# Performance work log

Hardware: AMD Instinct MI355X
Metric: run time of the kernel (lower is better)

The kernel has to match this reference:

```python
import jax, jax.numpy as jnp
import numpy as np

D_MODEL = 1024
NUM_HEADS = 16
D_HEAD = D_MODEL // NUM_HEADS
THETA = 10000.0
NEG_INF = -1e9


def apply_rope(x, theta=THETA):
    # x: (..., S, Dh) with interleaved pairs (2i, 2i+1)
    S, Dh = x.shape[-2], x.shape[-1]
    inv_freq = 1.0 / (theta ** (jnp.arange(0, Dh, 2, dtype=jnp.float32) / Dh))  # (Dh/2,)
    ang = jnp.arange(S, dtype=jnp.float32)[:, None] * inv_freq[None, :]          # (S, Dh/2)
    cos, sin = jnp.cos(ang), jnp.sin(ang)
    x1 = x[..., 0::2]
    x2 = x[..., 1::2]
    r1 = x1 * cos - x2 * sin
    r2 = x1 * sin + x2 * cos
    # interleave back
    return jnp.stack([r1, r2], axis=-1).reshape(x.shape)


def setup_inputs() -> dict:
    key = jax.random.key(0)
    ks = jax.random.split(key, 5)
    B, S = 2, 2048
    scale = 1.0 / np.sqrt(D_MODEL)
    return {
        "x": jax.random.normal(ks[0], (B, S, D_MODEL), dtype=jnp.float32),
        "Wq": jax.random.normal(ks[1], (D_MODEL, D_MODEL), dtype=jnp.float32) * scale,
        "Wk": jax.random.normal(ks[2], (D_MODEL, D_MODEL), dtype=jnp.float32) * scale,
        "Wv": jax.random.normal(ks[3], (D_MODEL, D_MODEL), dtype=jnp.float32) * scale,
        "Wo": jax.random.normal(ks[4], (D_MODEL, D_MODEL), dtype=jnp.float32) * scale,
    }


def reference(x, Wq, Wk, Wv, Wo):
    B, S, _ = x.shape
    def split_heads(t):
        return t.reshape(B, S, NUM_HEADS, D_HEAD).transpose(0, 2, 1, 3)  # (B,H,S,Dh)
    # nn.Linear(bias=False): y = x @ W.T
    Q = split_heads(x @ Wq.T)
    K = split_heads(x @ Wk.T)
    V = split_heads(x @ Wv.T)
    Q = apply_rope(Q)
    K = apply_rope(K)
    scale = 1.0 / jnp.sqrt(jnp.asarray(D_HEAD, dtype=x.dtype))
    scores = jnp.einsum("bhqd,bhkd->bhqk", Q, K) * scale  # (B,H,S,S)
    causal = jnp.tril(jnp.ones((S, S), dtype=bool))
    scores = jnp.where(causal, scores, NEG_INF)
    attn = jax.nn.softmax(scores, axis=-1)
    out = jnp.einsum("bhqk,bhkd->bhqd", attn, V)
    out = out.transpose(0, 2, 1, 3).reshape(B, S, D_MODEL)
    return out @ Wo.T
```

## Files before the change

kernel.cpp:

```cpp
#include <hip/hip_runtime.h>
#include <hip/hip_bf16.h>
#include <stdint.h>

typedef __attribute__((ext_vector_type(8))) short bf8;
typedef __attribute__((ext_vector_type(4))) float f4;
typedef __attribute__((ext_vector_type(16))) float f16f;
typedef __attribute__((ext_vector_type(4))) unsigned int u32x4;

#define MFMA16(a, b, c) __builtin_amdgcn_mfma_f32_16x16x32_bf16((a), (b), (c), 0, 0, 0)
#define MFMA32(a, b, c) __builtin_amdgcn_mfma_f32_32x32x16_bf16((a), (b), (c), 0, 0, 0)

static __device__ __forceinline__ short f2b(float f) {
  uint32_t x = __float_as_uint(f);
  x += 0x7fffu + ((x >> 16) & 1u);
  return (short)(x >> 16);
}

static __device__ __forceinline__ uint32_t cvtpk(float lo, float hi) {
  uint32_t r;
  asm("v_cvt_pk_bf16_f32 %0, %1, %2" : "=v"(r) : "v"(lo), "v"(hi));
  return r;
}

static __device__ __forceinline__ bf8 mk_bf8(uint32_t w0, uint32_t w1,
                                             uint32_t w2, uint32_t w3) {
  union { u32x4 u; bf8 b; } t;
  t.u = (u32x4){w0, w1, w2, w3};
  return t.b;
}

static __device__ __forceinline__ void gload16(const short* g, void* l) {
  __builtin_amdgcn_global_load_lds(
      (const __attribute__((address_space(1))) void*)g,
      (__attribute__((address_space(3))) void*)l, 16, 0, 0);
}

__global__ void convert_kernel(const float* __restrict__ x,
                               const float* __restrict__ wq, const float* __restrict__ wk,
                               const float* __restrict__ wv, const float* __restrict__ wo,
                               short* __restrict__ xb, short* __restrict__ Wb,
                               float2* __restrict__ tab) {
  const int bid = blockIdx.x;
  if (bid >= 4096) {
    const int t = (bid - 4096) * 256 + threadIdx.x;
    const int s = t >> 5, i = t & 31;
    const float inv = powf(10000.0f, -(float)i * (1.0f / 32.0f));
    const float ang = (float)s * inv;
    float sv, cv;
    sincosf(ang, &sv, &cv);
    tab[t] = make_float2(cv, sv);
    return;
  }
  const size_t i = ((size_t)bid * 256 + threadIdx.x) * 8;
  const float* __restrict__ src;
  short* __restrict__ dst;
  if (i < 4194304u) {
    src = x + i;
    dst = xb + i;
  } else {
    const size_t j = i - 4194304u;
    const int z = (int)(j >> 20);
    const size_t o = j & 1048575u;
    src = (z == 0 ? wq : z == 1 ? wk : z == 2 ? wv : wo) + o;
    dst = Wb + j;
  }
  const float4 a = *(const float4*)src;
  const float4 b = *(const float4*)(src + 4);
  bf8 v;
  v[0] = f2b(a.x); v[1] = f2b(a.y); v[2] = f2b(a.z); v[3] = f2b(a.w);
  v[4] = f2b(b.x); v[5] = f2b(b.y); v[6] = f2b(b.z); v[7] = f2b(b.w);
  *(bf8*)dst = v;
}

template <int MODE>
__launch_bounds__(256, 2)
__global__ void gemm_kernel(const short* __restrict__ Ab, const short* __restrict__ Wb,
                            short* __restrict__ Qo, short* __restrict__ Ko,
                            short* __restrict__ VTo, float* __restrict__ Fo,
                            const float2* __restrict__ rope) {
  constexpr int K = 1024;
  const int bm = blockIdx.x, bn = blockIdx.y;
  const int z = (MODE == 0) ? blockIdx.z : 3;
  const short* __restrict__ Bb = Wb + ((size_t)z << 20);

  __shared__ short As[128 * 64];
  __shared__ short Bs[128 * 64];

  const int tid = threadIdx.x;
  const int lane = tid & 63;
  const int wave = tid >> 6;
  const int wr = wave >> 1, wc = wave & 1;
  const int lg = lane >> 4, lr = lane & 15;

  f4 acc[4][4];
#pragma unroll
  for (int i = 0; i < 4; i++)
#pragma unroll
    for (int j = 0; j < 4; j++) {
      acc[i][j][0] = 0.f; acc[i][j][1] = 0.f;
      acc[i][j][2] = 0.f; acc[i][j][3] = 0.f;
    }

  const int kc = tid & 7;
  const int srow = tid >> 3;
  const int kcs = (kc ^ (srow & 7)) * 8;
  char* const Asw = (char*)As + wave * 1024;
  char* const Bsw = (char*)Bs + wave * 1024;

  for (int k0 = 0; k0 < K; k0 += 64) {
#pragma unroll
    for (int i = 0; i < 4; i++) {
      const int row = srow + i * 32;
      gload16(Ab + (size_t)(bm * 128 + row) * K + k0 + kcs, Asw + i * 4096);
      gload16(Bb + (size_t)(bn * 128 + row) * K + k0 + kcs, Bsw + i * 4096);
    }
    __syncthreads();
#pragma unroll
    for (int kk = 0; kk < 2; kk++) {
      bf8 af[4], bb[4];
#pragma unroll
      for (int mi = 0; mi < 4; mi++) {
        const int row = wr * 64 + mi * 16 + lr;
        const int lb = (row * 128 + kk * 64 + lg * 16) ^ ((row & 7) << 4);
        af[mi] = *(const bf8*)((const char*)As + lb);
      }
#pragma unroll
      for (int ni = 0; ni < 4; ni++) {
        const int row = wc * 64 + ni * 16 + lr;
        const int lb = (row * 128 + kk * 64 + lg * 16) ^ ((row & 7) << 4);
        bb[ni] = *(const bf8*)((const char*)Bs + lb);
      }
#pragma unroll
      for (int mi = 0; mi < 4; mi++)
#pragma unroll
        for (int ni = 0; ni < 4; ni++)
          acc[mi][ni] = MFMA16(af[mi], bb[ni], acc[mi][ni]);
    }
    __syncthreads();
  }

  if (MODE == 1) {
#pragma unroll
    for (int mi = 0; mi < 4; mi++) {
      const int m0 = bm * 128 + wr * 64 + mi * 16 + lg * 4;
#pragma unroll
      for (int ni = 0; ni < 4; ni++) {
        const int n = bn * 128 + wc * 64 + ni * 16 + lr;
#pragma unroll
        for (int r = 0; r < 4; r++)
          Fo[(size_t)(m0 + r) * 1024 + n] = acc[mi][ni][r];
      }
    }
    return;
  }

  if (z == 2) {
#pragma unroll
    for (int mi = 0; mi < 4; mi++) {
      const int m0 = bm * 128 + wr * 64 + mi * 16 + lg * 4;
      const int b = m0 >> 11, s0 = m0 & 2047;
#pragma unroll
      for (int ni = 0; ni < 4; ni++) {
        const int n = bn * 128 + wc * 64 + ni * 16 + lr;
        const int h = n >> 6, d = n & 63;
        ushort4 pk;
        pk.x = (unsigned short)f2b(acc[mi][ni][0]);
        pk.y = (unsigned short)f2b(acc[mi][ni][1]);
        pk.z = (unsigned short)f2b(acc[mi][ni][2]);
        pk.w = (unsigned short)f2b(acc[mi][ni][3]);
        ((ushort4*)VTo)[((size_t)(b * 16 + h) * 32 + (s0 >> 6)) * 1024 +
                        (((s0 & 63) >> 2) << 6) + d] = pk;
      }
    }
  } else {
    const float qscale = (z == 0) ? 0.18033688011112042f : 1.0f;
#pragma unroll
    for (int mi = 0; mi < 4; mi++) {
      const int m0 = bm * 128 + wr * 64 + mi * 16 + lg * 4;
      const int b = m0 >> 11, s0 = m0 & 2047;
#pragma unroll
      for (int ni = 0; ni < 4; ni++) {
        const int n = bn * 128 + wc * 64 + ni * 16 + lr;
        const int h = n >> 6, d = n & 63;
        const float sgn = (d & 1) ? 1.0f : -1.0f;
#pragma unroll
        for (int r = 0; r < 4; r++) {
          const float v = acc[mi][ni][r];
          const float p = __shfl_xor(v, 1);
          const int s = s0 + r;
          const float2 cs = rope[(s << 5) + (d >> 1)];
          const short res = f2b((v * cs.x + sgn * p * cs.y) * qscale);
          if (z == 0) {
            Qo[((size_t)(b * 16 + h) * 2048 + s) * 64 + d] = res;
          } else {
            Ko[(((size_t)(b * 16 + h) * 32 + (s >> 6)) << 12) +
               ((((d >> 3) << 6) + (s & 63)) << 3) + (d & 7)] = res;
          }
        }
      }
    }
  }
}

__launch_bounds__(256, 2)
__global__ void attn_kernel(const short* __restrict__ Qg, const short* __restrict__ K2,
                            const short* __restrict__ V2, short* __restrict__ AO) {
  const int id = blockIdx.x;
  const int xcd = id & 7;
  const int rest = id >> 3;
  const int bh = xcd * 4 + (rest & 3);
  const int j = 15 - (rest >> 2);
  const int tid = threadIdx.x;
  const int lane = tid & 63, wave = tid >> 6;
  const int l31 = lane & 31, hi = lane >> 5;
  const short* __restrict__ Qp = Qg + ((size_t)bh << 17);
  const short* __restrict__ KR = K2 + ((size_t)bh << 17);
  const short* __restrict__ VR = V2 + ((size_t)bh << 17);

  __shared__ short KB[2][2][4096];
  __shared__ short VB[2][2][4096];

  const int t = 4 * j + wave;
  const int qbase = t << 5;
  const int nR = j + 1;

#define STG(buf, kb_)                                                             \
  do {                                                                            \
    _Pragma("unroll") for (int h_ = 0; h_ < 2; h_++) {                            \
      const short* kr_ = KR + ((size_t)((kb_) * 2 + h_) << 12);                   \
      const short* vr_ = VR + ((size_t)((kb_) * 2 + h_) << 12);                   \
      gload16(kr_ + (size_t)(wave * 64 + lane) * 8, (char*)KB[buf][h_] + wave * 1024);          \
      gload16(kr_ + (size_t)(256 + wave * 64 + lane) * 8, (char*)KB[buf][h_] + 4096 + wave * 1024); \
      gload16(vr_ + (size_t)(wave * 64 + lane) * 8, (char*)VB[buf][h_] + wave * 1024);          \
      gload16(vr_ + (size_t)(256 + wave * 64 + lane) * 8, (char*)VB[buf][h_] + 4096 + wave * 1024); \
    }                                                                             \
  } while (0)

  bf8 qf[4];
#pragma unroll
  for (int ks = 0; ks < 4; ks++)
    qf[ks] = *(const bf8*)(Qp + (size_t)(qbase + l31) * 64 + ks * 16 + hi * 8);

  f16f o0, o1;
#pragma unroll
  for (int i = 0; i < 16; i++) { o0[i] = 0.f; o1[i] = 0.f; }
  float mrun = -1e30f, lsum = 0.f;

  STG(0, 0);
  __syncthreads();

  for (int kb = 0; kb < nR; kb++) {
    const int cur = kb & 1;

    if (kb + 1 < nR) STG(cur ^ 1, kb + 1);

#pragma unroll
    for (int h = 0; h < 2; h++) {
      const int kvbh = kb * 128 + 64 * h;
      if (kvbh < qbase + 32) {
        const char* Kc = (const char*)KB[cur][h];
        const char* Vc = (const char*)VB[cur][h];

        f16f st0, st1;
#pragma unroll
        for (int i = 0; i < 16; i++) { st0[i] = 0.f; st1[i] = 0.f; }
        __builtin_amdgcn_s_setprio(1);
#pragma unroll
        for (int ks = 0; ks < 4; ks++) {
          const bf8 k0f = *(const bf8*)(Kc + (2 * ks + hi) * 1024 + l31 * 16);
          const bf8 k1f = *(const bf8*)(Kc + (2 * ks + hi) * 1024 + (32 + l31) * 16);
          st0 = MFMA32(k0f, qf[ks], st0);
          st1 = MFMA32(k1f, qf[ks], st1);
        }
        __builtin_amdgcn_s_setprio(0);

        if (kvbh + 63 > qbase) {
          const int q = qbase + l31;
#pragma unroll
          for (int reg = 0; reg < 16; reg++) {
            const int kv = kvbh + (reg & 3) + 8 * (reg >> 2) + 4 * hi;
            if (kv > q) st0[reg] = -1e9f;
            if (kv + 32 > q) st1[reg] = -1e9f;
          }
        }

        float m0 = fmaxf(st0[0], st1[0]);
#pragma unroll
        for (int reg = 1; reg < 16; reg++) m0 = fmaxf(m0, fmaxf(st0[reg], st1[reg]));

        if (__any(m0 - mrun > 8.0f)) {
          m0 = fmaxf(m0, __shfl_xor(m0, 32));
          const float mn = fmaxf(mrun, m0);
          const float corr = __builtin_amdgcn_exp2f(mrun - mn);
          mrun = mn;
          lsum *= corr;
#pragma unroll
          for (int reg = 0; reg < 16; reg++) {
            const int qo = (reg & 3) + 8 * (reg >> 2) + 4 * hi;
            const float co = __shfl(corr, qo);
            o0[reg] *= co;
            o1[reg] *= co;
          }
        }

#pragma unroll
        for (int reg = 0; reg < 16; reg++) {
          st0[reg] = __builtin_amdgcn_exp2f(st0[reg] - mrun);
          st1[reg] = __builtin_amdgcn_exp2f(st1[reg] - mrun);
          lsum += st0[reg] + st1[reg];
        }

        bf8 pa[4];
#pragma unroll
        for (int k2 = 0; k2 < 4; k2++) {
          const f16f& pn = (k2 < 2) ? st0 : st1;
          const int bs = (k2 & 1) * 8;
          uint32_t x0 = cvtpk(pn[bs + 0], pn[bs + 1]);
          uint32_t y0 = cvtpk(pn[bs + 4], pn[bs + 5]);
          uint32_t x1 = cvtpk(pn[bs + 2], pn[bs + 3]);
          uint32_t y1 = cvtpk(pn[bs + 6], pn[bs + 7]);
          asm volatile("v_permlane32_swap_b32 %0, %1" : "+v"(x0), "+v"(y0));
          asm volatile("v_permlane32_swap_b32 %0, %1" : "+v"(x1), "+v"(y1));
          pa[k2] = mk_bf8(x0, x1, y0, y1);
        }

        __builtin_amdgcn_s_setprio(1);
#pragma unroll
        for (int k2 = 0; k2 < 4; k2++) {
          const int Jb = ((4 * k2 + 2 * hi) * 64 + l31) * 8;
          const uint2 a0 = *(const uint2*)(Vc + Jb);
          const uint2 a1 = *(const uint2*)(Vc + Jb + 512);
          const uint2 b0 = *(const uint2*)(Vc + Jb + 256);
          const uint2 b1 = *(const uint2*)(Vc + Jb + 768);
          const bf8 v0 = mk_bf8(a0.x, a0.y, a1.x, a1.y);
          const bf8 v1 = mk_bf8(b0.x, b0.y, b1.x, b1.y);
          o0 = MFMA32(pa[k2], v0, o0);
          o1 = MFMA32(pa[k2], v1, o1);
        }
        __builtin_amdgcn_s_setprio(0);
      }
    }

    __syncthreads();
  }

  const float s = lsum + __shfl_xor(lsum, 32);
  const float inv = 1.0f / s;
  const int b = bh >> 4, h = bh & 15;
#pragma unroll
  for (int reg = 0; reg < 16; reg++) {
    const int qo = (reg & 3) + 8 * (reg >> 2) + 4 * hi;
    const float io = __shfl(inv, qo);
    const int q = qbase + qo;
    const size_t base = ((size_t)b * 2048 + q) * 1024 + h * 64 + l31;
    AO[base] = f2b(o0[reg] * io);
    AO[base + 32] = f2b(o1[reg] * io);
  }
#undef STG
}

extern "C" void kernel_launch(void* const* d_in, const int* in_sizes, int n_in,
                              void* d_out, int out_size, void* d_ws, size_t ws_size,
                              hipStream_t stream) {
  const float* x  = (const float*)d_in[0];
  const float* wq = (const float*)d_in[1];
  const float* wk = (const float*)d_in[2];
  const float* wv = (const float*)d_in[3];
  const float* wo = (const float*)d_in[4];
  float* out = (float*)d_out;

  char* ws = (char*)d_ws;
  short*  Qb  = (short*)(ws);
  short*  Kb  = (short*)(ws + (8ull  << 20));
  short*  VTb = (short*)(ws + (16ull << 20));
  short*  AOb = (short*)(ws + (24ull << 20));
  short*  xb  = AOb;
  short*  Wb  = (short*)(ws + (32ull << 20));
  float2* tab = (float2*)(ws + (40ull << 20));

  convert_kernel<<<4352, 256, 0, stream>>>(x, wq, wk, wv, wo, xb, Wb, tab);
  gemm_kernel<0><<<dim3(32, 8, 3), 256, 0, stream>>>(
      xb, Wb, Qb, Kb, VTb, nullptr, tab);
  attn_kernel<<<512, 256, 0, stream>>>(Qb, Kb, VTb, AOb);
  gemm_kernel<1><<<dim3(32, 8, 1), 256, 0, stream>>>(
      AOb, Wb, nullptr, nullptr, nullptr, out, nullptr);
}
```

Measured before the change: 114.1 us.

## Use plain K/V-transposed layouts and 8-wave attention blocks with direct LDS staging

The QKV GEMM epilogue now writes K in the same plain row-major per-head layout as Q, and V as a plain per-head transpose (d-major, s contiguous), instead of the earlier pre-tiled layouts. The attention kernel switches to 512-thread blocks covering 256 queries each, launches 256 blocks, and stages 64x64 K/V tiles straight from those plain layouts into the same LDS arrangement. V fragments are now read as single 16-byte LDS loads instead of being assembled from four 8-byte loads. The aim is fewer, larger blocks, more K/V reuse per staged tile, and simpler GEMM stores. In exchange, the V stores in the GEMM become strided across rows. The launch bound of 512 threads with 4 blocks per CU also caps registers per thread tightly, which risks spills.

```diff
diff --git a/kernel.cpp b/kernel.cpp
--- a/kernel.cpp
+++ b/kernel.cpp
@@ -162,17 +162,16 @@
 #pragma unroll
       for (int ni = 0; ni < 4; ni++) {
         const int n = bn * 128 + wc * 64 + ni * 16 + lr;
-        const int h = n >> 6, d = n & 63;
         ushort4 pk;
         pk.x = (unsigned short)f2b(acc[mi][ni][0]);
         pk.y = (unsigned short)f2b(acc[mi][ni][1]);
         pk.z = (unsigned short)f2b(acc[mi][ni][2]);
         pk.w = (unsigned short)f2b(acc[mi][ni][3]);
-        ((ushort4*)VTo)[((size_t)(b * 16 + h) * 32 + (s0 >> 6)) * 1024 +
-                        (((s0 & 63) >> 2) << 6) + d] = pk;
+        *(ushort4*)(VTo + ((size_t)((b * 16 + (n >> 6)) * 64 + (n & 63))) * 2048 + s0) = pk;
       }
     }
   } else {
+    short* __restrict__ Out = (z == 0) ? Qo : Ko;
     const float qscale = (z == 0) ? 0.18033688011112042f : 1.0f;
 #pragma unroll
     for (int mi = 0; mi < 4; mi++) {
@@ -187,53 +186,46 @@
         for (int r = 0; r < 4; r++) {
           const float v = acc[mi][ni][r];
           const float p = __shfl_xor(v, 1);
-          const int s = s0 + r;
-          const float2 cs = rope[(s << 5) + (d >> 1)];
-          const short res = f2b((v * cs.x + sgn * p * cs.y) * qscale);
-          if (z == 0) {
-            Qo[((size_t)(b * 16 + h) * 2048 + s) * 64 + d] = res;
-          } else {
-            Ko[(((size_t)(b * 16 + h) * 32 + (s >> 6)) << 12) +
-               ((((d >> 3) << 6) + (s & 63)) << 3) + (d & 7)] = res;
-          }
-        }
-      }
-    }
-  }
-}
-
-__launch_bounds__(256, 2)
-__global__ void attn_kernel(const short* __restrict__ Qg, const short* __restrict__ K2,
-                            const short* __restrict__ V2, short* __restrict__ AO) {
+          const float2 cs = rope[((s0 + r) << 5) + (d >> 1)];
+          const float res = (v * cs.x + sgn * p * cs.y) * qscale;
+          Out[((size_t)(b * 16 + h) * 2048 + (s0 + r)) * 64 + d] = f2b(res);
+        }
+      }
+    }
+  }
+}
+
+__launch_bounds__(512, 4)
+__global__ void attn_kernel(const short* __restrict__ Qg, const short* __restrict__ Kg,
+                            const short* __restrict__ Vg, short* __restrict__ AO) {
   const int id = blockIdx.x;
   const int xcd = id & 7;
   const int rest = id >> 3;
   const int bh = xcd * 4 + (rest & 3);
-  const int j = 15 - (rest >> 2);
+  const int j = 7 - (rest >> 2);
   const int tid = threadIdx.x;
   const int lane = tid & 63, wave = tid >> 6;
   const int l31 = lane & 31, hi = lane >> 5;
   const short* __restrict__ Qp = Qg + ((size_t)bh << 17);
-  const short* __restrict__ KR = K2 + ((size_t)bh << 17);
-  const short* __restrict__ VR = V2 + ((size_t)bh << 17);
+  const short* __restrict__ Kp = Kg + ((size_t)bh << 17);
+  const short* __restrict__ Vp = Vg + ((size_t)bh << 17);
 
   __shared__ short KB[2][2][4096];
   __shared__ short VB[2][2][4096];
 
-  const int t = 4 * j + wave;
+  const int t = 8 * j + wave;
   const int qbase = t << 5;
-  const int nR = j + 1;
-
-#define STG(buf, kb_)                                                             \
-  do {                                                                            \
-    _Pragma("unroll") for (int h_ = 0; h_ < 2; h_++) {                            \
-      const short* kr_ = KR + ((size_t)((kb_) * 2 + h_) << 12);                   \
-      const short* vr_ = VR + ((size_t)((kb_) * 2 + h_) << 12);                   \
-      gload16(kr_ + (size_t)(wave * 64 + lane) * 8, (char*)KB[buf][h_] + wave * 1024);          \
-      gload16(kr_ + (size_t)(256 + wave * 64 + lane) * 8, (char*)KB[buf][h_] + 4096 + wave * 1024); \
-      gload16(vr_ + (size_t)(wave * 64 + lane) * 8, (char*)VB[buf][h_] + wave * 1024);          \
-      gload16(vr_ + (size_t)(256 + wave * 64 + lane) * 8, (char*)VB[buf][h_] + 4096 + wave * 1024); \
-    }                                                                             \
+  const int blkR = 2 * j + 2;
+
+#define STG(buf, kb_)                                                            \
+  do {                                                                           \
+    _Pragma("unroll") for (int h_ = 0; h_ < 2; h_++) {                           \
+      const int kvb_ = (kb_) * 128 + 64 * h_;                                    \
+      gload16(Kp + (size_t)(kvb_ + lane) * 64 + wave * 8,                        \
+              (char*)KB[buf][h_] + wave * 1024);                                 \
+      gload16(Vp + (size_t)lane * 2048 + kvb_ + wave * 8,                        \
+              (char*)VB[buf][h_] + wave * 1024);                                 \
+    }                                                                            \
   } while (0)
 
   bf8 qf[4];
@@ -249,10 +241,10 @@
   STG(0, 0);
   __syncthreads();
 
-  for (int kb = 0; kb < nR; kb++) {
+  for (int kb = 0; kb < blkR; kb++) {
     const int cur = kb & 1;
 
-    if (kb + 1 < nR) STG(cur ^ 1, kb + 1);
+    if (kb + 1 < blkR) STG(cur ^ 1, kb + 1);
 
 #pragma unroll
     for (int h = 0; h < 2; h++) {
@@ -268,7 +260,7 @@
 #pragma unroll
         for (int ks = 0; ks < 4; ks++) {
           const bf8 k0f = *(const bf8*)(Kc + (2 * ks + hi) * 1024 + l31 * 16);
-          const bf8 k1f = *(const bf8*)(Kc + (2 * ks + hi) * 1024 + (32 + l31) * 16);
+          const bf8 k1f = *(const bf8*)(Kc + (2 * ks + hi) * 1024 + 512 + l31 * 16);
           st0 = MFMA32(k0f, qf[ks], st0);
           st1 = MFMA32(k1f, qf[ks], st1);
         }
@@ -327,13 +319,8 @@
         __builtin_amdgcn_s_setprio(1);
 #pragma unroll
         for (int k2 = 0; k2 < 4; k2++) {
-          const int Jb = ((4 * k2 + 2 * hi) * 64 + l31) * 8;
-          const uint2 a0 = *(const uint2*)(Vc + Jb);
-          const uint2 a1 = *(const uint2*)(Vc + Jb + 512);
-          const uint2 b0 = *(const uint2*)(Vc + Jb + 256);
-          const uint2 b1 = *(const uint2*)(Vc + Jb + 768);
-          const bf8 v0 = mk_bf8(a0.x, a0.y, a1.x, a1.y);
-          const bf8 v1 = mk_bf8(b0.x, b0.y, b1.x, b1.y);
+          const bf8 v0 = *(const bf8*)(Vc + (2 * k2 + hi) * 1024 + l31 * 16);
+          const bf8 v1 = *(const bf8*)(Vc + (2 * k2 + hi) * 1024 + 512 + l31 * 16);
           o0 = MFMA32(pa[k2], v0, o0);
           o1 = MFMA32(pa[k2], v1, o1);
         }
@@ -381,7 +368,7 @@
   convert_kernel<<<4352, 256, 0, stream>>>(x, wq, wk, wv, wo, xb, Wb, tab);
   gemm_kernel<0><<<dim3(32, 8, 3), 256, 0, stream>>>(
       xb, Wb, Qb, Kb, VTb, nullptr, tab);
-  attn_kernel<<<512, 256, 0, stream>>>(Qb, Kb, VTb, AOb);
+  attn_kernel<<<256, 512, 0, stream>>>(Qb, Kb, VTb, AOb);
   gemm_kernel<1><<<dim3(32, 8, 1), 256, 0, stream>>>(
       AOb, Wb, nullptr, nullptr, nullptr, out, nullptr);
 }
```

Result: slower. 125.1 us (+9.7%).
